# Kernel optimization log

Hardware: AMD Instinct MI355X
Metric: run time of the kernel (lower is better)

## Reference

```python
import jax, jax.numpy as jnp
import numpy as np

B, TT, TA, H = 2, 128, 512, 1024
EPS = 1e-5


def _conv1d(x, w, b, pad):
    # x: [B, C_in, T], w: [C_out, C_in, K] -> [B, C_out, T]
    y = jax.lax.conv_general_dilated(x, w, window_strides=(1,), padding=[(pad, pad)],
                                     dimension_numbers=('NCH', 'OIH', 'NCH'))
    return y + b[None, :, None]


def _groupnorm1(x, g, b):
    # GroupNorm(num_groups=1): normalize over (C, T) per sample. x: [B, C, T]
    mu = jnp.mean(x, axis=(1, 2), keepdims=True)
    var = jnp.var(x, axis=(1, 2), keepdims=True)
    xn = (x - mu) * jax.lax.rsqrt(var + EPS)
    return xn * g[None, :, None] + b[None, :, None]


def setup_inputs() -> dict:
    key = jax.random.key(0)
    ks = jax.random.split(key, 16)
    s = 0.02
    return {
        'text_hidden': jax.random.normal(ks[0], (B, TT, H), jnp.float32),
        'audio_hidden': jax.random.normal(ks[1], (B, TA, H), jnp.float32),
        # alignment_proj: Linear(2H, H) -> ReLU -> Linear(H, 1)
        'a_w1': jax.random.normal(ks[2], (2 * H, H), jnp.float32) * s,
        'a_b1': jnp.zeros((H,), jnp.float32),
        'a_w2': jax.random.normal(ks[3], (H, 1), jnp.float32) * s,
        'a_b2': jnp.zeros((1,), jnp.float32),
        # duration_predictor: Conv1d(H,H,3) ReLU GN(1,H) Conv1d(H,H,3) ReLU GN(1,H) Conv1d(H,1,1)
        'd_w1': jax.random.normal(ks[4], (H, H, 3), jnp.float32) * s,
        'd_b1': jnp.zeros((H,), jnp.float32),
        'gn1_g': jnp.ones((H,), jnp.float32),
        'gn1_b': jnp.zeros((H,), jnp.float32),
        'd_w2': jax.random.normal(ks[5], (H, H, 3), jnp.float32) * s,
        'd_b2': jnp.zeros((H,), jnp.float32),
        'gn2_g': jnp.ones((H,), jnp.float32),
        'gn2_b': jnp.zeros((H,), jnp.float32),
        'd_w3': jax.random.normal(ks[6], (1, H, 1), jnp.float32) * s,
        'd_b3': jnp.zeros((1,), jnp.float32),
    }


def reference(text_hidden, audio_hidden, a_w1, a_b1, a_w2, a_b2,
              d_w1, d_b1, gn1_g, gn1_b, d_w2, d_b2, gn2_g, gn2_b, d_w3, d_b3):
    # ---- predict_durations ----
    x = jnp.swapaxes(text_hidden, 1, 2)                      # [B, H, TT]
    x = _groupnorm1(jax.nn.relu(_conv1d(x, d_w1, d_b1, 1)), gn1_g, gn1_b)
    x = _groupnorm1(jax.nn.relu(_conv1d(x, d_w2, d_b2, 1)), gn2_g, gn2_b)
    x = _conv1d(x, d_w3, d_b3, 0)                            # [B, 1, TT]
    durations = jax.nn.softplus(x[:, 0, :])                  # [B, TT]

    # ---- soft_mas (temperature = 1.0) ----
    # Linear on concat([text, audio]) == text @ W1[:H] + audio @ W1[H:] + b1
    t_part = jnp.einsum('bth,hd->btd', text_hidden, a_w1[:H])    # [B, TT, H]
    a_part = jnp.einsum('bah,hd->bad', audio_hidden, a_w1[H:])   # [B, TA, H]
    hid = jax.nn.relu(t_part[:, :, None, :] + a_part[:, None, :, :] + a_b1)  # [B,TT,TA,H]
    logits = jnp.einsum('btad,do->bta', hid, a_w2) + a_b2[0]     # [B, TT, TA]

    pos = jnp.arange(TA, dtype=logits.dtype)                     # audio positions j
    expected = jnp.arange(TT, dtype=logits.dtype) * (TA / TT)    # expected pos per text i
    monotonic_bias = -0.1 * jnp.abs(pos[None, :] - expected[:, None])  # [TT, TA]
    logits = logits + monotonic_bias[None, :, :]

    alignment = jax.nn.softmax(logits, axis=-1)
    return alignment, durations
```

## Files before the change

kernel.cpp:

```cpp
#include <hip/hip_runtime.h>
#include <hip/hip_bf16.h>


typedef __bf16 bf16_t;
typedef __bf16 bf16x8 __attribute__((ext_vector_type(8)));
typedef __bf16 bf16x4 __attribute__((ext_vector_type(4)));
typedef float  f32x4  __attribute__((ext_vector_type(4)));
typedef _Float16 f16_t;
typedef _Float16 f16x2 __attribute__((ext_vector_type(2)));
typedef _Float16 f16x4 __attribute__((ext_vector_type(4)));
typedef int v4i __attribute__((ext_vector_type(4)));

#define EPSV 1e-5f

#define GLD(dst, ptr, off) \
    asm volatile("global_load_dwordx4 %0, %1, off offset:%c2" \
                 : "=v"(dst) : "v"(ptr), "n"(off) : "memory")
#define WAITV(n) do { \
    asm volatile("s_waitcnt vmcnt(%c0)" :: "n"(n) : "memory"); \
    __builtin_amdgcn_sched_barrier(0); } while (0)

__device__ __forceinline__ bf16x8 as_bf16x8(v4i v) {
    union { v4i i; bf16x8 h; } u; u.i = v; return u.h;
}

__device__ __forceinline__ void pair_store16(bf16_t* even_addr, bf16x4 v, int t) {
    union { bf16x4 h; unsigned u[2]; } a; a.h = v;
    const unsigned ox = __shfl_down(a.u[0], 1);
    const unsigned oy = __shfl_down(a.u[1], 1);
    if (!(t & 1)) {
        union { unsigned u[4]; v4i i; } o;
        o.u[0] = a.u[0]; o.u[1] = a.u[1]; o.u[2] = ox; o.u[3] = oy;
        *(v4i*)even_addr = o.i;
    }
}

#define OFF_TEXTP    0u
#define OFF_AUDIOP   524288u
#define OFF_W1TOP    2621440u
#define OFF_W1BOT    4718592u
#define OFF_WC1      6815744u
#define OFF_WC2      13107200u
#define OFF_TP       19398656u
#define OFF_W2F      19922944u
#define OFF_APT      20447232u
#define OFF_XP0      22544384u
#define OFF_XP1      23076864u
#define OFF_Y2       23609344u
#define OFF_BST1     24133632u
#define OFF_BST2     24137728u
#define OFF_LP       24141824u
#define OFF_SG       26238976u
#define OFF_SB       26251264u
#define OFF_SGF      26263552u
#define OFF_SBF      26267648u

__global__ __launch_bounds__(256) void prep_k(
    const float* __restrict__ text, const float* __restrict__ audio,
    const float* __restrict__ w1,
    const float* __restrict__ w1c, const float* __restrict__ w2,
    bf16_t* __restrict__ textP, bf16_t* __restrict__ xp0,
    bf16_t* __restrict__ audioP,
    bf16_t* __restrict__ topP, bf16_t* __restrict__ botP,
    bf16_t* __restrict__ wc1,
    bf16_t* __restrict__ xp1, f16_t* __restrict__ w2f)
{
    __shared__ float tile[32][33];
    const int bid = blockIdx.x;
    const int tid = threadIdx.x;
    if (bid < 1280) {
        const int e = (bid * 256 + tid) * 4;
        if (e < 262144) {
            float4 v = *(const float4*)&text[e];
            bf16x4 o; o[0] = (bf16_t)v.x; o[1] = (bf16_t)v.y; o[2] = (bf16_t)v.z; o[3] = (bf16_t)v.w;
            const int bt = e >> 10, h = e & 1023;
            const int b = bt >> 7, t = bt & 127;
            *(bf16x4*)&xp0[(size_t)(b * 130 + 1 + t) * 1024 + h] = o;
            const int h0 = h & ~7;
            const int lane = (bt & 15) | (((h0 >> 3) & 3) << 4);
            bf16_t* ea = &textP[((size_t)((bt >> 4) * 32 + (h0 >> 5))) * 512 + lane * 8];
            pair_store16(ea, o, tid);
        } else {
            const int ea4 = e - 262144;
            float4 v = *(const float4*)&audio[ea4];
            bf16x4 o; o[0] = (bf16_t)v.x; o[1] = (bf16_t)v.y; o[2] = (bf16_t)v.z; o[3] = (bf16_t)v.w;
            const int ba = ea4 >> 10, h = ea4 & 1023;
            const int h0 = h & ~7;
            const int lane = (ba & 15) | (((h0 >> 3) & 3) << 4);
            bf16_t* ea = &audioP[((size_t)((ba >> 4) * 32 + (h0 >> 5))) * 512 + lane * 8];
            pair_store16(ea, o, tid);
        }
    } else if (bid < 3328) {
        const int b2 = bid - 1280;
        const int bx = b2 & 31, by = b2 >> 5;
        const int tx = tid & 31, ty = tid >> 5;
        #pragma unroll
        for (int j = 0; j < 4; ++j)
            tile[ty + j * 8][tx] = w1[(size_t)(by * 32 + ty + j * 8) * 1024 + bx * 32 + tx];
        __syncthreads();
        if (tid < 128) {
            const int rbl = tid >> 6, lane = tid & 63;
            const int dl = rbl * 16 + (lane & 15);
            const int lkp = lane >> 4;
            bf16x8 v8;
            #pragma unroll
            for (int e2 = 0; e2 < 8; ++e2) v8[e2] = (bf16_t)tile[lkp * 8 + e2][dl];
            const int d = bx * 32 + dl;
            bf16_t* out = (by < 32) ? topP : botP;
            *(bf16x8*)&out[((size_t)((d >> 4) * 32 + (by & 31))) * 512 + lane * 8] = v8;
        }
    } else if (bid < 4352) {
        const int o = bid - 3328;
        const int i0 = tid * 4;
        const float* src = w1c + (size_t)o * 3072 + tid * 12;
        float4 v0 = *(const float4*)&src[0];
        float4 v1 = *(const float4*)&src[4];
        float4 v2 = *(const float4*)&src[8];
        const float f[12] = {v0.x, v0.y, v0.z, v0.w, v1.x, v1.y, v1.z, v1.w, v2.x, v2.y, v2.z, v2.w};
        const int ip = i0 & ~7;
        const int lane = (o & 15) | (((ip >> 3) & 3) << 4);
        #pragma unroll
        for (int r = 0; r < 3; ++r) {
            bf16x4 o4;
            #pragma unroll
            for (int j = 0; j < 4; ++j) o4[j] = (bf16_t)f[j * 3 + r];
            bf16_t* ea = &wc1[((size_t)(r * 2048 + (o >> 4) * 32 + (ip >> 5))) * 512 + lane * 8];
            pair_store16(ea, o4, tid);
        }
    } else {
        const int rowmap[4] = {0, 129, 130, 259};
        const int f = tid * 16;
        const int r = f >> 10, w = f & 1023;
        bf16x8 z8 = (bf16x8)(bf16_t)0.0f;
        bf16_t* p0 = xp0 + (size_t)rowmap[r] * 1024 + w;
        bf16_t* p1 = xp1 + (size_t)rowmap[r] * 1024 + w;
        *(bf16x8*)p0 = z8; *(bf16x8*)(p0 + 8) = z8;
        *(bf16x8*)p1 = z8; *(bf16x8*)(p1 + 8) = z8;
        float4 wv = *(const float4*)&w2[tid * 4];
        f16x4 wo; wo[0] = (f16_t)wv.x; wo[1] = (f16_t)wv.y; wo[2] = (f16_t)wv.z; wo[3] = (f16_t)wv.w;
        *(f16x4*)&w2f[tid * 4] = wo;
    }
}

__device__ __forceinline__ float wave_red_add(float v) {
    #pragma unroll
    for (int off = 32; off > 0; off >>= 1) v += __shfl_xor(v, off);
    return v;
}

__device__ __forceinline__ void conv_body(
    const bf16_t* __restrict__ WcP, const bf16_t* __restrict__ xp,
    int by, int b, int tbase, int w, int l, bf16_t* Bs, int tid,
    f32x4& acc0, f32x4& acc1)
{
    const int lm = l & 15, lk = (l >> 4) * 8;
    const bf16_t* xrow = xp + (size_t)(b * 130 + tbase) * 1024;
    #pragma unroll 1
    for (int c = 0; c < 4; ++c) {
        __syncthreads();
        const int kc = c * 8 + w;
        const bf16_t* a0 = WcP + ((size_t)(by * 32 + kc)) * 512 + l * 8;
        v4i A0, A1, A2;
        GLD(A0, a0, 0);
        GLD(A1, a0 + 1048576, 0);
        GLD(A2, a0 + 2097152, 0);
        for (int idx = tid; idx < 1088; idx += 512) {
            const int row = idx >> 5, col = (idx & 31) * 8;
            *(v4i*)&Bs[row * 264 + col] =
                *(const v4i*)&xrow[(size_t)row * 1024 + c * 256 + col];
        }
        __syncthreads();
        const int cb = w * 32 + lk;
        bf16x8 b00 = *(const bf16x8*)&Bs[(lm + 0) * 264 + cb];
        bf16x8 b10 = *(const bf16x8*)&Bs[(lm + 16) * 264 + cb];
        bf16x8 b01 = *(const bf16x8*)&Bs[(lm + 1) * 264 + cb];
        bf16x8 b11 = *(const bf16x8*)&Bs[(lm + 17) * 264 + cb];
        bf16x8 b02 = *(const bf16x8*)&Bs[(lm + 2) * 264 + cb];
        bf16x8 b12 = *(const bf16x8*)&Bs[(lm + 18) * 264 + cb];
        WAITV(2);
        acc0 = __builtin_amdgcn_mfma_f32_16x16x32_bf16(as_bf16x8(A0), b00, acc0, 0, 0, 0);
        acc1 = __builtin_amdgcn_mfma_f32_16x16x32_bf16(as_bf16x8(A0), b10, acc1, 0, 0, 0);
        WAITV(1);
        acc0 = __builtin_amdgcn_mfma_f32_16x16x32_bf16(as_bf16x8(A1), b01, acc0, 0, 0, 0);
        acc1 = __builtin_amdgcn_mfma_f32_16x16x32_bf16(as_bf16x8(A1), b11, acc1, 0, 0, 0);
        WAITV(0);
        acc0 = __builtin_amdgcn_mfma_f32_16x16x32_bf16(as_bf16x8(A2), b02, acc0, 0, 0, 0);
        acc1 = __builtin_amdgcn_mfma_f32_16x16x32_bf16(as_bf16x8(A2), b12, acc1, 0, 0, 0);
    }
    __syncthreads();
}

__global__ __launch_bounds__(512) void p2_k(
    const bf16_t* __restrict__ wc1, const bf16_t* __restrict__ xp0,
    const float* __restrict__ d_b1, bf16_t* __restrict__ xp1,
    float* __restrict__ bstat1,
    const bf16_t* __restrict__ textP, const bf16_t* __restrict__ topP,
    const float* __restrict__ a_b1, f16_t* __restrict__ tp,
    const bf16_t* __restrict__ audioP, const bf16_t* __restrict__ botP,
    f16_t* __restrict__ apT4,
    const float* __restrict__ w2c, const float* __restrict__ g1,
    const float* __restrict__ b1g, bf16_t* __restrict__ wc2,
    float* __restrict__ Sg3, float* __restrict__ Sb3,
    float* __restrict__ SgF, float* __restrict__ SbF)
{
    __shared__ float smem[8448];
    __shared__ float sred[8], sredq[8];
    const int bid = blockIdx.x;
    const int tid = threadIdx.x;
    const int w = tid >> 6, l = tid & 63;
    const int lm = l & 15, lh = l >> 4;
    if (bid < 512) {
        const int bx = bid >> 6, by = bid & 63;
        const int bt0 = bx * 32, m0 = by * 16;
        const int b = bt0 >> 7, tbase = bt0 & 127;
        f32x4 acc0 = (f32x4)(0.0f), acc1 = (f32x4)(0.0f);
        conv_body(wc1, xp0, by, b, tbase, w, l, (bf16_t*)smem, tid, acc0, acc1);
        float* sl = smem + w * 528;
        #pragma unroll
        for (int r = 0; r < 4; ++r) {
            sl[(lh * 4 + r) * 33 + lm] = acc0[r];
            sl[(lh * 4 + r) * 33 + 16 + lm] = acc1[r];
        }
        __syncthreads();
        const int mm = tid >> 5, nn = tid & 31;
        float v = 0.f;
        #pragma unroll
        for (int ww = 0; ww < 8; ++ww) v += smem[ww * 528 + mm * 33 + nn];
        v = fmaxf(v + d_b1[m0 + mm], 0.f);
        float s = wave_red_add(v), q = wave_red_add(v * v);
        if (l == 0) { sred[w] = s; sredq[w] = q; }
        xp1[(size_t)(b * 130 + 1 + tbase + nn) * 1024 + m0 + mm] = (bf16_t)v;
        __syncthreads();
        if (tid == 0) {
            float ts = 0.f, tq = 0.f;
            #pragma unroll
            for (int ww = 0; ww < 8; ++ww) { ts += sred[ww]; tq += sredq[ww]; }
            bstat1[bid * 2] = ts; bstat1[bid * 2 + 1] = tq;
        }
    } else if (bid < 1792) {
        const bf16_t *At, *Bm;
        int d0, r0, is_tp;
        if (bid < 768) {
            const int unit = bid - 512;
            d0 = (unit & 31) * 32; r0 = (unit >> 5) * 32;
            At = topP; Bm = textP; is_tp = 1;
        } else {
            const int unit = bid - 768;
            d0 = (unit & 31) * 32; r0 = (unit >> 5) * 32;
            At = botP; Bm = audioP; is_tp = 0;
        }
        const int rb0 = d0 >> 4, rbB = r0 >> 4;
        const bf16_t* Ap0 = At + ((size_t)(rb0 * 32 + w * 4)) * 512 + l * 8;
        const bf16_t* Ap1 = Ap0 + 16384;
        const bf16_t* Bp0 = Bm + ((size_t)(rbB * 32 + w * 4)) * 512 + l * 8;
        const bf16_t* Bp1 = Bp0 + 16384;
        v4i qa0[4], qa1[4], qb0[4], qb1[4];
        GLD(qa0[0], Ap0,    0); GLD(qa1[0], Ap1,    0); GLD(qb0[0], Bp0,    0); GLD(qb1[0], Bp1,    0);
        GLD(qa0[1], Ap0, 1024); GLD(qa1[1], Ap1, 1024); GLD(qb0[1], Bp0, 1024); GLD(qb1[1], Bp1, 1024);
        GLD(qa0[2], Ap0, 2048); GLD(qa1[2], Ap1, 2048); GLD(qb0[2], Bp0, 2048); GLD(qb1[2], Bp1, 2048);
        GLD(qa0[3], Ap0, 3072); GLD(qa1[3], Ap1, 3072); GLD(qb0[3], Bp0, 3072); GLD(qb1[3], Bp1, 3072);
        f32x4 acc[2][2];
        #pragma unroll
        for (int mt = 0; mt < 2; ++mt)
            #pragma unroll
            for (int nt = 0; nt < 2; ++nt) acc[mt][nt] = (f32x4)(0.0f);
#define GMF(cc, n) \
        WAITV(n); \
        acc[0][0] = __builtin_amdgcn_mfma_f32_16x16x32_bf16(as_bf16x8(qa0[cc]), as_bf16x8(qb0[cc]), acc[0][0], 0, 0, 0); \
        acc[0][1] = __builtin_amdgcn_mfma_f32_16x16x32_bf16(as_bf16x8(qa0[cc]), as_bf16x8(qb1[cc]), acc[0][1], 0, 0, 0); \
        acc[1][0] = __builtin_amdgcn_mfma_f32_16x16x32_bf16(as_bf16x8(qa1[cc]), as_bf16x8(qb0[cc]), acc[1][0], 0, 0, 0); \
        acc[1][1] = __builtin_amdgcn_mfma_f32_16x16x32_bf16(as_bf16x8(qa1[cc]), as_bf16x8(qb1[cc]), acc[1][1], 0, 0, 0)
        GMF(0, 12); GMF(1, 8); GMF(2, 4); GMF(3, 0);
#undef GMF
        float* sl = smem + w * 1056;
        #pragma unroll
        for (int mt = 0; mt < 2; ++mt)
            #pragma unroll
            for (int nt = 0; nt < 2; ++nt)
                #pragma unroll
                for (int r = 0; r < 4; ++r)
                    sl[(mt * 16 + lh * 4 + r) * 33 + nt * 16 + lm] = acc[mt][nt][r];
        __syncthreads();
        const int m = tid >> 4, n2 = (tid & 15) * 2;
        float v0 = 0.f, v1 = 0.f;
        #pragma unroll
        for (int ww = 0; ww < 8; ++ww) {
            v0 += smem[ww * 1056 + m * 33 + n2];
            v1 += smem[ww * 1056 + m * 33 + n2 + 1];
        }
        if (is_tp) {
            const float bb = a_b1[d0 + m];
            tp[(size_t)(r0 + n2) * 1024 + d0 + m] = (f16_t)(v0 + bb);
            tp[(size_t)(r0 + n2 + 1) * 1024 + d0 + m] = (f16_t)(v1 + bb);
        } else {
            const int h = d0 + m, hq = h >> 2, hr = h & 3;
            const int a0 = r0 + n2;
            const int bbk = a0 >> 9, al = a0 & 511;
            apT4[((size_t)hq * 1024 + bbk * 512 + al) * 4 + hr] = (f16_t)v0;
            apT4[((size_t)hq * 1024 + bbk * 512 + al + 1) * 4 + hr] = (f16_t)v1;
        }
    } else {
        const int half = tid >> 8, t = tid & 255;
        const int o = (bid - 1792) * 2 + half;
        const int i0 = t * 4;
        const float* src = w2c + (size_t)o * 3072 + t * 12;
        float4 v0 = *(const float4*)&src[0];
        float4 v1 = *(const float4*)&src[4];
        float4 v2 = *(const float4*)&src[8];
        const float f[12] = {v0.x, v0.y, v0.z, v0.w, v1.x, v1.y, v1.z, v1.w, v2.x, v2.y, v2.z, v2.w};
        float4 gv = *(const float4*)&g1[i0];
        float4 bv = *(const float4*)&b1g[i0];
        const float g4[4] = {gv.x, gv.y, gv.z, gv.w};
        const float bb4[4] = {bv.x, bv.y, bv.z, bv.w};
        const int ip = i0 & ~7;
        const int lane = (o & 15) | (((ip >> 3) & 3) << 4);
        float sgr[3] = {0.f, 0.f, 0.f}, sbr[3] = {0.f, 0.f, 0.f};
        #pragma unroll
        for (int r = 0; r < 3; ++r) {
            bf16x4 o4;
            #pragma unroll
            for (int j = 0; j < 4; ++j) {
                const float wv = f[j * 3 + r];
                const float ws = wv * g4[j];
                sgr[r] += ws;
                sbr[r] += wv * bb4[j];
                o4[j] = (bf16_t)ws;
            }
            bf16_t* ea = &wc2[((size_t)(r * 2048 + (o >> 4) * 32 + (ip >> 5))) * 512 + lane * 8];
            pair_store16(ea, o4, t);
        }
        #pragma unroll
        for (int off = 32; off > 0; off >>= 1) {
            #pragma unroll
            for (int r = 0; r < 3; ++r) {
                sgr[r] += __shfl_xor(sgr[r], off);
                sbr[r] += __shfl_xor(sbr[r], off);
            }
        }
        float* red = smem + half * 32;
        const int wid = t >> 6, lane2 = t & 63;
        if (lane2 == 0) {
            #pragma unroll
            for (int r = 0; r < 3; ++r) {
                red[wid * 6 + r] = sgr[r];
                red[wid * 6 + 3 + r] = sbr[r];
            }
        }
        __syncthreads();
        if (t < 6) {
            const float v = red[t] + red[6 + t] + red[12 + t] + red[18 + t];
            if (t < 3) Sg3[o * 3 + t] = v;
            else       Sb3[o * 3 + t - 3] = v;
            red[24 + t] = v;
        }
        __syncthreads();
        if (t == 0)      SgF[o] = red[24] + red[25] + red[26];
        else if (t == 1) SbF[o] = red[27] + red[28] + red[29];
    }
}

__device__ __forceinline__ void reduce_bstat(
    const float* __restrict__ bstat, int b, int tid,
    float* sr, float* sq, float& mu, float& rsig)
{
    const int lane = tid & 63, wid = tid >> 6;
    float s = 0.f, q = 0.f;
    if (tid < 256) {
        float2 v = ((const float2*)bstat)[b * 256 + tid];
        s = v.x; q = v.y;
    }
    #pragma unroll
    for (int off = 32; off > 0; off >>= 1) {
        s += __shfl_xor(s, off);
        q += __shfl_xor(q, off);
    }
    if (lane == 0) { sr[wid] = s; sq[wid] = q; }
    __syncthreads();
    float ts = 0.f, tq = 0.f;
    #pragma unroll
    for (int i = 0; i < 8; ++i) { ts += sr[i]; tq += sq[i]; }
    const float cnt = 131072.f;
    mu = ts / cnt;
    const float var = tq / cnt - mu * mu;
    rsig = rsqrtf(var + EPSV);
}

__device__ __forceinline__ float dot2_acc(f16x2 x, f16x2 w, float acc) {
#if __has_builtin(__builtin_amdgcn_fdot2)
    return __builtin_amdgcn_fdot2(x, w, acc, false);
#else
    return acc + (float)x[0] * (float)w[0] + (float)x[1] * (float)w[1];
#endif
}

__global__ __launch_bounds__(512) void p3_k(
    const bf16_t* __restrict__ wc2, const bf16_t* __restrict__ xp1,
    const float* __restrict__ d_b2, bf16_t* __restrict__ y2,
    float* __restrict__ bstat2, const float* __restrict__ bstat1,
    const float* __restrict__ SgF, const float* __restrict__ SbF,
    const float* __restrict__ Sg3, const float* __restrict__ Sb3,
    const f16_t* __restrict__ tp, const f16_t* __restrict__ apT4,
    const f16_t* __restrict__ w2f, float* __restrict__ lp)
{
    __shared__ float smem[4608];
    __shared__ float sred[8], sredq[8], sr[8], sq[8];
    const int bid = blockIdx.x;
    const int tid = threadIdx.x;
    if (bid < 512) {
        const int w = tid >> 6, l = tid & 63;
        const int lm = l & 15, lh = l >> 4;
        const int bx = bid >> 6, by = bid & 63;
        const int bt0 = bx * 32, m0 = by * 16;
        const int b = bt0 >> 7, tbase = bt0 & 127;
        f32x4 acc0 = (f32x4)(0.0f), acc1 = (f32x4)(0.0f);
        conv_body(wc2, xp1, by, b, tbase, w, l, (bf16_t*)smem, tid, acc0, acc1);
        float* sl = smem + w * 528;
        #pragma unroll
        for (int r = 0; r < 4; ++r) {
            sl[(lh * 4 + r) * 33 + lm] = acc0[r];
            sl[(lh * 4 + r) * 33 + 16 + lm] = acc1[r];
        }
        __syncthreads();
        const int mm = tid >> 5, nn = tid & 31;
        float vraw = 0.f;
        #pragma unroll
        for (int ww = 0; ww < 8; ++ww) vraw += smem[ww * 528 + mm * 33 + nn];
        float mu, rsig;
        reduce_bstat(bstat1, b, tid, sr, sq, mu, rsig);
        const int o = m0 + mm, tloc = tbase + nn;
        float sg = SgF[o], sb = SbF[o];
        if (tloc == 0)   { sg -= Sg3[o * 3];     sb -= Sb3[o * 3]; }
        if (tloc == 127) { sg -= Sg3[o * 3 + 2]; sb -= Sb3[o * 3 + 2]; }
        float v = fmaxf(rsig * vraw + sb - mu * rsig * sg + d_b2[o], 0.f);
        float s = wave_red_add(v), q = wave_red_add(v * v);
        if ((tid & 63) == 0) { sred[tid >> 6] = s; sredq[tid >> 6] = q; }
        y2[(size_t)(b * 128 + tloc) * 1024 + o] = (bf16_t)v;
        __syncthreads();
        if (tid == 0) {
            float ts = 0.f, tq = 0.f;
            #pragma unroll
            for (int ww = 0; ww < 8; ++ww) { ts += sred[ww]; tq += sredq[ww]; }
            bstat2[bid * 2] = ts; bstat2[bid * 2 + 1] = tq;
        }
    } else {
        const int lb = bid - 512;
        const int hc = lb >> 6, btp = lb & 63;
        const int bt0 = btp * 4;
        const int b = bt0 >> 7;
        const int a = tid;
        const f16_t* tpr = tp + (size_t)bt0 * 1024 + hc * 256;
        const f16_t* w2r = w2f + hc * 256;
        const f16_t* apc = apT4 + ((size_t)(hc * 64) * 1024 + b * 512 + a) * 4;
        float acc[4] = {0.f, 0.f, 0.f, 0.f};
        const f16x2 zero = (f16x2)(f16_t)0.0f;
#define L_A0(i) (*(const f16x4*)(apc + (size_t)(2 * (i)) * 4096))
#define L_A1(i) (*(const f16x4*)(apc + (size_t)(2 * (i) + 1) * 4096))
        constexpr int PF = 4;
        f16x4 pa[PF], pb[PF];
        #pragma unroll
        for (int i = 0; i < PF; ++i) { pa[i] = L_A0(i); pb[i] = L_A1(i); }
        #pragma unroll
        for (int i = 0; i < 32; ++i) {
            const int sl = i % PF;
            const int hq = 2 * i;
            f16x4 a0 = pa[sl], a1 = pb[sl];
            f16x4 w0 = *(const f16x4*)&w2r[hq * 4];
            f16x4 w1 = *(const f16x4*)&w2r[hq * 4 + 4];
            #pragma unroll
            for (int r = 0; r < 4; ++r) {
                f16x4 t0 = *(const f16x4*)&tpr[r * 1024 + hq * 4];
                f16x4 t1 = *(const f16x4*)&tpr[r * 1024 + hq * 4 + 4];
                f16x2 p;
                p = __builtin_elementwise_max((f16x2){t0[0] + a0[0], t0[1] + a0[1]}, zero);
                acc[r] = dot2_acc(p, (f16x2){w0[0], w0[1]}, acc[r]);
                p = __builtin_elementwise_max((f16x2){t0[2] + a0[2], t0[3] + a0[3]}, zero);
                acc[r] = dot2_acc(p, (f16x2){w0[2], w0[3]}, acc[r]);
                p = __builtin_elementwise_max((f16x2){t1[0] + a1[0], t1[1] + a1[1]}, zero);
                acc[r] = dot2_acc(p, (f16x2){w1[0], w1[1]}, acc[r]);
                p = __builtin_elementwise_max((f16x2){t1[2] + a1[2], t1[3] + a1[3]}, zero);
                acc[r] = dot2_acc(p, (f16x2){w1[2], w1[3]}, acc[r]);
            }
            const int nx = i + PF;
            if (nx < 32) { pa[sl] = L_A0(nx); pb[sl] = L_A1(nx); }
        }
#undef L_A0
#undef L_A1
        float* dst = lp + (size_t)(hc * 256 + bt0) * 512 + a;
        #pragma unroll
        for (int r = 0; r < 4; ++r) dst[(size_t)r * 512] = acc[r];
    }
}

__global__ __launch_bounds__(512) void combine_k(
    const float* __restrict__ lp, const float* __restrict__ b2,
    const bf16_t* __restrict__ y2, const float* __restrict__ bstat2,
    const float* __restrict__ g, const float* __restrict__ bet,
    const float* __restrict__ w3, const float* __restrict__ b3,
    float* __restrict__ out)
{
    __shared__ float redm[8], redsum[8];
    const int bid = blockIdx.x;
    const int tid = threadIdx.x;
    if (bid < 256) {
        const int bt = bid, t = bt & 127;
        const int a = tid;
        const int lane = a & 63, wid = a >> 6;
        const size_t base = (size_t)bt * 512 + a;
        float v = lp[base] + lp[131072 + base] + lp[262144 + base] + lp[393216 + base];
        v += b2[0] - 0.1f * fabsf((float)a - 4.0f * (float)t);
        float m = v;
        #pragma unroll
        for (int off = 32; off > 0; off >>= 1) m = fmaxf(m, __shfl_xor(m, off));
        if (lane == 0) redm[wid] = m;
        __syncthreads();
        float M = redm[0];
        #pragma unroll
        for (int i = 1; i < 8; ++i) M = fmaxf(M, redm[i]);
        const float e = expf(v - M);
        float s = e;
        #pragma unroll
        for (int off = 32; off > 0; off >>= 1) s += __shfl_xor(s, off);
        if (lane == 0) redsum[wid] = s;
        __syncthreads();
        float S = redsum[0];
        #pragma unroll
        for (int i = 1; i < 8; ++i) S += redsum[i];
        out[(size_t)bt * 512 + a] = e * (1.0f / S);
    } else {
        const int cb = bid - 256;
        const int b = (cb * 8) >> 7;
        float mu, rsig;
        reduce_bstat(bstat2, b, tid, redm, redsum, mu, rsig);
        const int lane = tid & 63, w = tid >> 6;
        const int bt = cb * 8 + w;
        const bf16_t* row = y2 + (size_t)bt * 1024 + lane * 16;
        float s1 = 0.f, s2 = 0.f, s3 = 0.f;
        #pragma unroll
        for (int c = 0; c < 2; ++c) {
            bf16x8 yv = *(const bf16x8*)(row + c * 8);
            #pragma unroll
            for (int j = 0; j < 8; ++j) {
                const int i = lane * 16 + c * 8 + j;
                const float gw = g[i] * w3[i];
                s1 += gw * (float)yv[j];
                s2 += gw;
                s3 += bet[i] * w3[i];
            }
        }
        #pragma unroll
        for (int off = 32; off > 0; off >>= 1) {
            s1 += __shfl_xor(s1, off);
            s2 += __shfl_xor(s2, off);
            s3 += __shfl_xor(s3, off);
        }
        if (lane == 0) {
            const float t = rsig * (s1 - mu * s2) + s3 + b3[0];
            out[131072 + bt] = fmaxf(t, 0.f) + log1pf(expf(-fabsf(t)));
        }
    }
}

extern "C" void kernel_launch(void* const* d_in, const int* in_sizes, int n_in,
                              void* d_out, int out_size, void* d_ws, size_t ws_size,
                              hipStream_t stream) {
    const float* text   = (const float*)d_in[0];
    const float* audio  = (const float*)d_in[1];
    const float* a_w1   = (const float*)d_in[2];
    const float* a_b1   = (const float*)d_in[3];
    const float* a_w2   = (const float*)d_in[4];
    const float* a_b2   = (const float*)d_in[5];
    const float* d_w1   = (const float*)d_in[6];
    const float* d_b1   = (const float*)d_in[7];
    const float* gn1_g  = (const float*)d_in[8];
    const float* gn1_b  = (const float*)d_in[9];
    const float* d_w2   = (const float*)d_in[10];
    const float* d_b2   = (const float*)d_in[11];
    const float* gn2_g  = (const float*)d_in[12];
    const float* gn2_b  = (const float*)d_in[13];
    const float* d_w3   = (const float*)d_in[14];
    const float* d_b3   = (const float*)d_in[15];

    char* ws = (char*)d_ws;
    float* outf = (float*)d_out;

    bf16_t* textP    = (bf16_t*)(ws + OFF_TEXTP);
    bf16_t* audioP   = (bf16_t*)(ws + OFF_AUDIOP);
    bf16_t* topP     = (bf16_t*)(ws + OFF_W1TOP);
    bf16_t* botP     = (bf16_t*)(ws + OFF_W1BOT);
    bf16_t* wc1      = (bf16_t*)(ws + OFF_WC1);
    bf16_t* wc2      = (bf16_t*)(ws + OFF_WC2);
    f16_t*  tp       = (f16_t*) (ws + OFF_TP);
    f16_t*  w2f      = (f16_t*) (ws + OFF_W2F);
    f16_t*  apT4     = (f16_t*) (ws + OFF_APT);
    bf16_t* xp0      = (bf16_t*)(ws + OFF_XP0);
    bf16_t* xp1      = (bf16_t*)(ws + OFF_XP1);
    bf16_t* y2       = (bf16_t*)(ws + OFF_Y2);
    float*  bstat1   = (float*) (ws + OFF_BST1);
    float*  bstat2   = (float*) (ws + OFF_BST2);
    float*  lp       = (float*) (ws + OFF_LP);
    float*  Sg3      = (float*) (ws + OFF_SG);
    float*  Sb3      = (float*) (ws + OFF_SB);
    float*  SgFp     = (float*) (ws + OFF_SGF);
    float*  SbFp     = (float*) (ws + OFF_SBF);

    prep_k<<<dim3(4353), 256, 0, stream>>>(text, audio, a_w1, d_w1, a_w2,
                                           textP, xp0, audioP, topP, botP,
                                           wc1, xp1, w2f);
    p2_k<<<dim3(2304), 512, 0, stream>>>(wc1, xp0, d_b1, xp1, bstat1,
                                         textP, topP, a_b1, tp,
                                         audioP, botP, apT4,
                                         d_w2, gn1_g, gn1_b, wc2,
                                         Sg3, Sb3, SgFp, SbFp);
    p3_k<<<dim3(768), 512, 0, stream>>>(wc2, xp1, d_b2, y2, bstat2, bstat1,
                                        SgFp, SbFp, Sg3, Sb3, tp, apT4, w2f, lp);
    combine_k<<<dim3(288), 512, 0, stream>>>(lp, a_b2, y2, bstat2,
                                             gn2_g, gn2_b, d_w3, d_b3, outf);
}
```

Baseline: 150.7 us.

## Fuse alignment logit reduction and softmax into p3 blocks, dropping partial-sum buffer

Each alignment block in p3 now covers the full hidden dimension instead of a quarter of it. It applies bias, the monotonic bias and the row softmax in-block and writes the alignment output directly. This removes the fp32 partial-logit workspace round trip and the softmax branch of combine_k, which now only computes durations. The alignment grid shrinks from 256 to 64 blocks, each doing four times longer serial work. That lowers parallelism and may lengthen the critical path of p3.

```diff
diff --git a/kernel.cpp b/kernel.cpp
--- a/kernel.cpp
+++ b/kernel.cpp
@@ -49,7 +49,6 @@
 #define OFF_Y2       23609344u
 #define OFF_BST1     24133632u
 #define OFF_BST2     24137728u
-#define OFF_LP       24141824u
 #define OFF_SG       26238976u
 #define OFF_SB       26251264u
 #define OFF_SGF      26263552u
@@ -400,10 +399,12 @@
     const float* __restrict__ SgF, const float* __restrict__ SbF,
     const float* __restrict__ Sg3, const float* __restrict__ Sb3,
     const f16_t* __restrict__ tp, const f16_t* __restrict__ apT4,
-    const f16_t* __restrict__ w2f, float* __restrict__ lp)
+    const f16_t* __restrict__ w2f, const float* __restrict__ ab2,
+    float* __restrict__ out)
 {
     __shared__ float smem[4608];
     __shared__ float sred[8], sredq[8], sr[8], sq[8];
+    __shared__ float redm[32], redsum[32];
     const int bid = blockIdx.x;
     const int tid = threadIdx.x;
     if (bid < 512) {
@@ -443,14 +444,13 @@
             bstat2[bid * 2] = ts; bstat2[bid * 2 + 1] = tq;
         }
     } else {
-        const int lb = bid - 512;
-        const int hc = lb >> 6, btp = lb & 63;
+        const int btp = bid - 512;
         const int bt0 = btp * 4;
-        const int b = bt0 >> 7;
+        const int b = bt0 >> 7, tbase = bt0 & 127;
         const int a = tid;
-        const f16_t* tpr = tp + (size_t)bt0 * 1024 + hc * 256;
-        const f16_t* w2r = w2f + hc * 256;
-        const f16_t* apc = apT4 + ((size_t)(hc * 64) * 1024 + b * 512 + a) * 4;
+        const int lane = tid & 63, wid = tid >> 6;
+        const f16_t* tpr = tp + (size_t)bt0 * 1024;
+        const f16_t* apc = apT4 + ((size_t)(b * 512 + a)) * 4;
         float acc[4] = {0.f, 0.f, 0.f, 0.f};
         const f16x2 zero = (f16x2)(f16_t)0.0f;
 #define L_A0(i) (*(const f16x4*)(apc + (size_t)(2 * (i)) * 4096))
@@ -459,13 +459,13 @@
         f16x4 pa[PF], pb[PF];
         #pragma unroll
         for (int i = 0; i < PF; ++i) { pa[i] = L_A0(i); pb[i] = L_A1(i); }
-        #pragma unroll
-        for (int i = 0; i < 32; ++i) {
+        #pragma unroll 2
+        for (int i = 0; i < 128; ++i) {
             const int sl = i % PF;
             const int hq = 2 * i;
             f16x4 a0 = pa[sl], a1 = pb[sl];
-            f16x4 w0 = *(const f16x4*)&w2r[hq * 4];
-            f16x4 w1 = *(const f16x4*)&w2r[hq * 4 + 4];
+            f16x4 w0 = *(const f16x4*)&w2f[hq * 4];
+            f16x4 w1 = *(const f16x4*)&w2f[hq * 4 + 4];
             #pragma unroll
             for (int r = 0; r < 4; ++r) {
                 f16x4 t0 = *(const f16x4*)&tpr[r * 1024 + hq * 4];
@@ -481,82 +481,91 @@
                 acc[r] = dot2_acc(p, (f16x2){w1[2], w1[3]}, acc[r]);
             }
             const int nx = i + PF;
-            if (nx < 32) { pa[sl] = L_A0(nx); pb[sl] = L_A1(nx); }
+            if (nx < 128) { pa[sl] = L_A0(nx); pb[sl] = L_A1(nx); }
         }
 #undef L_A0
 #undef L_A1
-        float* dst = lp + (size_t)(hc * 256 + bt0) * 512 + a;
-        #pragma unroll
-        for (int r = 0; r < 4; ++r) dst[(size_t)r * 512] = acc[r];
+        const float b2v = ab2[0];
+        float vv[4], mx[4];
+        #pragma unroll
+        for (int r = 0; r < 4; ++r) {
+            vv[r] = acc[r] + b2v - 0.1f * fabsf((float)a - 4.0f * (float)(tbase + r));
+            mx[r] = vv[r];
+        }
+        #pragma unroll
+        for (int off = 32; off > 0; off >>= 1)
+            #pragma unroll
+            for (int r = 0; r < 4; ++r) mx[r] = fmaxf(mx[r], __shfl_xor(mx[r], off));
+        if (lane == 0) {
+            #pragma unroll
+            for (int r = 0; r < 4; ++r) redm[wid * 4 + r] = mx[r];
+        }
+        __syncthreads();
+        float M[4], ee[4], ss[4];
+        #pragma unroll
+        for (int r = 0; r < 4; ++r) {
+            M[r] = redm[r];
+            #pragma unroll
+            for (int i = 1; i < 8; ++i) M[r] = fmaxf(M[r], redm[i * 4 + r]);
+            ee[r] = expf(vv[r] - M[r]);
+            ss[r] = ee[r];
+        }
+        #pragma unroll
+        for (int off = 32; off > 0; off >>= 1)
+            #pragma unroll
+            for (int r = 0; r < 4; ++r) ss[r] += __shfl_xor(ss[r], off);
+        if (lane == 0) {
+            #pragma unroll
+            for (int r = 0; r < 4; ++r) redsum[wid * 4 + r] = ss[r];
+        }
+        __syncthreads();
+        #pragma unroll
+        for (int r = 0; r < 4; ++r) {
+            float S = redsum[r];
+            #pragma unroll
+            for (int i = 1; i < 8; ++i) S += redsum[i * 4 + r];
+            out[(size_t)(bt0 + r) * 512 + a] = ee[r] * (1.0f / S);
+        }
     }
 }
 
 __global__ __launch_bounds__(512) void combine_k(
-    const float* __restrict__ lp, const float* __restrict__ b2,
     const bf16_t* __restrict__ y2, const float* __restrict__ bstat2,
     const float* __restrict__ g, const float* __restrict__ bet,
     const float* __restrict__ w3, const float* __restrict__ b3,
     float* __restrict__ out)
 {
     __shared__ float redm[8], redsum[8];
-    const int bid = blockIdx.x;
+    const int cb = blockIdx.x;
     const int tid = threadIdx.x;
-    if (bid < 256) {
-        const int bt = bid, t = bt & 127;
-        const int a = tid;
-        const int lane = a & 63, wid = a >> 6;
-        const size_t base = (size_t)bt * 512 + a;
-        float v = lp[base] + lp[131072 + base] + lp[262144 + base] + lp[393216 + base];
-        v += b2[0] - 0.1f * fabsf((float)a - 4.0f * (float)t);
-        float m = v;
-        #pragma unroll
-        for (int off = 32; off > 0; off >>= 1) m = fmaxf(m, __shfl_xor(m, off));
-        if (lane == 0) redm[wid] = m;
-        __syncthreads();
-        float M = redm[0];
-        #pragma unroll
-        for (int i = 1; i < 8; ++i) M = fmaxf(M, redm[i]);
-        const float e = expf(v - M);
-        float s = e;
-        #pragma unroll
-        for (int off = 32; off > 0; off >>= 1) s += __shfl_xor(s, off);
-        if (lane == 0) redsum[wid] = s;
-        __syncthreads();
-        float S = redsum[0];
-        #pragma unroll
-        for (int i = 1; i < 8; ++i) S += redsum[i];
-        out[(size_t)bt * 512 + a] = e * (1.0f / S);
-    } else {
-        const int cb = bid - 256;
-        const int b = (cb * 8) >> 7;
-        float mu, rsig;
-        reduce_bstat(bstat2, b, tid, redm, redsum, mu, rsig);
-        const int lane = tid & 63, w = tid >> 6;
-        const int bt = cb * 8 + w;
-        const bf16_t* row = y2 + (size_t)bt * 1024 + lane * 16;
-        float s1 = 0.f, s2 = 0.f, s3 = 0.f;
-        #pragma unroll
-        for (int c = 0; c < 2; ++c) {
-            bf16x8 yv = *(const bf16x8*)(row + c * 8);
-            #pragma unroll
-            for (int j = 0; j < 8; ++j) {
-                const int i = lane * 16 + c * 8 + j;
-                const float gw = g[i] * w3[i];
-                s1 += gw * (float)yv[j];
-                s2 += gw;
-                s3 += bet[i] * w3[i];
-            }
-        }
-        #pragma unroll
-        for (int off = 32; off > 0; off >>= 1) {
-            s1 += __shfl_xor(s1, off);
-            s2 += __shfl_xor(s2, off);
-            s3 += __shfl_xor(s3, off);
-        }
-        if (lane == 0) {
-            const float t = rsig * (s1 - mu * s2) + s3 + b3[0];
-            out[131072 + bt] = fmaxf(t, 0.f) + log1pf(expf(-fabsf(t)));
-        }
+    const int b = (cb * 8) >> 7;
+    float mu, rsig;
+    reduce_bstat(bstat2, b, tid, redm, redsum, mu, rsig);
+    const int lane = tid & 63, w = tid >> 6;
+    const int bt = cb * 8 + w;
+    const bf16_t* row = y2 + (size_t)bt * 1024 + lane * 16;
+    float s1 = 0.f, s2 = 0.f, s3 = 0.f;
+    #pragma unroll
+    for (int c = 0; c < 2; ++c) {
+        bf16x8 yv = *(const bf16x8*)(row + c * 8);
+        #pragma unroll
+        for (int j = 0; j < 8; ++j) {
+            const int i = lane * 16 + c * 8 + j;
+            const float gw = g[i] * w3[i];
+            s1 += gw * (float)yv[j];
+            s2 += gw;
+            s3 += bet[i] * w3[i];
+        }
+    }
+    #pragma unroll
+    for (int off = 32; off > 0; off >>= 1) {
+        s1 += __shfl_xor(s1, off);
+        s2 += __shfl_xor(s2, off);
+        s3 += __shfl_xor(s3, off);
+    }
+    if (lane == 0) {
+        const float t = rsig * (s1 - mu * s2) + s3 + b3[0];
+        out[131072 + bt] = fmaxf(t, 0.f) + log1pf(expf(-fabsf(t)));
     }
 }
 
@@ -597,7 +606,6 @@
     bf16_t* y2       = (bf16_t*)(ws + OFF_Y2);
     float*  bstat1   = (float*) (ws + OFF_BST1);
     float*  bstat2   = (float*) (ws + OFF_BST2);
-    float*  lp       = (float*) (ws + OFF_LP);
     float*  Sg3      = (float*) (ws + OFF_SG);
     float*  Sb3      = (float*) (ws + OFF_SB);
     float*  SgFp     = (float*) (ws + OFF_SGF);
@@ -611,8 +619,9 @@
                                          audioP, botP, apT4,
                                          d_w2, gn1_g, gn1_b, wc2,
                                          Sg3, Sb3, SgFp, SbFp);
-    p3_k<<<dim3(768), 512, 0, stream>>>(wc2, xp1, d_b2, y2, bstat2, bstat1,
-                                        SgFp, SbFp, Sg3, Sb3, tp, apT4, w2f, lp);
-    combine_k<<<dim3(288), 512, 0, stream>>>(lp, a_b2, y2, bstat2,
-                                             gn2_g, gn2_b, d_w3, d_b3, outf);
-}
+    p3_k<<<dim3(576), 512, 0, stream>>>(wc2, xp1, d_b2, y2, bstat2, bstat1,
+                                        SgFp, SbFp, Sg3, Sb3, tp, apT4, w2f,
+                                        a_b2, outf);
+    combine_k<<<dim3(32), 512, 0, stream>>>(y2, bstat2,
+                                            gn2_g, gn2_b, d_w3, d_b3, outf);
+}
```

Result: slower. 505.0 us (+235.0%).
